# Kernel tuning notes

Hardware: AMD Instinct MI355X
Metric: run time of the kernel (lower is better)

Reference implementation:

```python
import jax, jax.numpy as jnp
import numpy as np
import math

B = 128      # bandwidth
BATCH = 2048 # flat batch (samples x channels)


def _dlt_weights(Bv):
    # Driscoll-Healy quadrature weights, length 2B
    k = np.arange(2 * Bv)
    p = np.arange(Bv)
    C = 2.0 / Bv * np.sin(np.pi * (2 * k + 1) / (4.0 * Bv))
    S = np.sin(np.outer(2 * k + 1, 2 * p + 1) * np.pi / (4.0 * Bv))  # [2B,B]
    return C * (S @ (1.0 / (2 * p + 1)))


def _idct_matrix(N):
    k = np.arange(N)[:, None]
    n = np.arange(N)[None, :]
    DI = np.cos(np.pi * n * (k + 0.5) / N)
    DI[:, 0] *= np.sqrt(1.0 / N)
    DI[:, 1:] *= np.sqrt(2.0 / N)
    return DI


def _idst_matrix(N):
    k = np.arange(N)[:, None]
    n = np.arange(N)[None, :]
    DI = np.sin(np.pi * (n + 1) * (k + 0.5) / N)
    DI[:, N - 1] = (-1.0) ** np.arange(N)
    DI[:, :N - 1] *= np.sqrt(2.0 / N)
    DI[:, N - 1] *= np.sqrt(1.0 / N)
    return DI


def _little_half(Bv):
    # Wigner little-d at beta=pi/2 via 3-term recurrence (vectorized over m,n)
    Bm1 = Bv - 1
    s2 = np.sqrt(2.0)
    d = np.zeros((Bv, 2 * Bv - 1, 2 * Bv - 1))
    d[0, Bm1, Bm1] = 1.0
    d[1, Bm1 - 1, Bm1 - 1] = 0.5
    d[1, Bm1 - 1, Bm1] = 1.0 / s2
    d[1, Bm1 - 1, Bm1 + 1] = 0.5
    d[1, Bm1, Bm1 - 1] = -1.0 / s2
    d[1, Bm1, Bm1 + 1] = 1.0 / s2
    d[1, Bm1 + 1, Bm1 - 1] = 0.5
    d[1, Bm1 + 1, Bm1] = -1.0 / s2
    d[1, Bm1 + 1, Bm1 + 1] = 0.5
    for l in range(2, Bv):
        m = np.arange(l).astype(np.float64)
        M, Nn = np.meshgrid(m, m, indexing='ij')
        denom = (l - 1.0) * np.sqrt((l - M) * (l + M) * (l - Nn) * (l + Nn))
        c1 = (1.0 - 2.0 * l) * M * Nn / denom
        c2 = -l * np.sqrt(((l - 1.0) ** 2 - M ** 2) * ((l - 1.0) ** 2 - Nn ** 2)) / denom
        d[l, Bm1:Bm1 + l, Bm1:Bm1 + l] = (c1 * d[l - 1, Bm1:Bm1 + l, Bm1:Bm1 + l]
                                          + c2 * d[l - 2, Bm1:Bm1 + l, Bm1:Bm1 + l])
        mm = np.arange(l + 1)
        lnV = np.array([0.5 * (math.lgamma(2 * l + 1) - math.lgamma(l + mi + 1)
                               - math.lgamma(l - mi + 1)) - l * math.log(2.0) for mi in mm])
        v = np.exp(lnV)
        d[l, Bm1 + mm, Bm1 + l] = v
        d[l, Bm1 + l, Bm1 + mm] = ((-1.0) ** (l - mm)) * v
        # symmetry fill (write order a1, a2, a3 reproduces torch loop semantics)
        sub = d[l, Bm1:Bm1 + l + 1, Bm1:Bm1 + l + 1].copy()
        M2, N2 = np.meshgrid(np.arange(l + 1), np.arange(l + 1), indexing='ij')
        a1 = ((-1.0) ** (M2 - N2)) * sub
        a2 = ((-1.0) ** (l - N2)) * sub
        a3 = ((-1.0) ** (l + M2)) * sub
        a1[0, 0] = sub[0, 0]
        a2[0, 0] = sub[0, 0]
        a3[0, 0] = sub[0, 0]
        d[l, Bm1 - l:Bm1 + 1, Bm1 - l:Bm1 + 1] = a1[::-1, ::-1]
        d[l, Bm1 - l:Bm1 + 1, Bm1:Bm1 + l + 1] = a2[::-1, :]
        d[l, Bm1:Bm1 + l + 1, Bm1 - l:Bm1 + 1] = a3[:, ::-1]
    return d


def _wigner_coeffs(Bv, d):
    Bm1 = Bv - 1
    N = 2 * Bv
    D = np.zeros((Bv, Bv, N))
    for m in range(Bv):
        for l in range(m, Bv):
            if m % 2 == 0:
                n = np.arange(l + 1)
                c = np.sqrt((2 * l + 1) / 2.0) * np.where(n == 0, np.sqrt(N), np.sqrt(2.0 * N))
                if m % 4 == 2:
                    c = -c
                coeff = c * d[l, n + Bm1, Bm1 - m] * d[l, n + Bm1, Bm1]
                coeff = np.where(np.abs(coeff) > 1e-15, coeff, 0.0)
                D[m, l, :l + 1] = coeff
            else:
                n = np.arange(l)  # n == l gives 0
                if l > 0:
                    c = np.sqrt((2 * l + 1) / 2.0) * np.sqrt(2.0 * N)
                    if m % 4 == 1:
                        c = -c
                    coeff = c * d[l, n + 1 + Bm1, Bm1 - m] * d[l, n + 1 + Bm1, Bm1]
                    coeff = np.where(np.abs(coeff) > 1e-15, coeff, 0.0)
                    D[m, l, :l] = coeff
    return D


def _buffers(Bv):
    N = 2 * Bv
    Wd = np.diag(_dlt_weights(Bv))
    XFc = Wd @ _idct_matrix(N)   # weighted DCT matrix (applied as x @ XFc)
    XFs = Wd @ _idst_matrix(N)   # weighted DST matrix
    D = _wigner_coeffs(Bv, _little_half(Bv))
    cm = ((-1.0) ** (Bv - 1)) * np.sqrt(1.0 / (2.0 * np.pi))  # Cm[B-1] scalar
    return XFc, XFs, D, cm


def setup_inputs() -> dict:
    key = jax.random.key(0)
    psiHat = jax.random.normal(key, (BATCH, B, 2 * B), dtype=jnp.float32)
    XFc, XFs, D, cm = _buffers(B)
    return {
        'psiHat': psiHat,
        'cm': jnp.float32(cm),
        'XFc': jnp.asarray(XFc, dtype=jnp.float32),
        'XFs': jnp.asarray(XFs, dtype=jnp.float32),
        'D': jnp.asarray(D, dtype=jnp.float32),
    }


def reference(psiHat, cm, XFc, XFs, D):
    # psiHat: [batch, B, 2B]; XFc/XFs: [2B, 2B]; D: [B, B, 2B]
    psi = psiHat * cm  # Cm[B-1:] broadcasts as a scalar
    # F.linear with weight = XF.T  ==  x @ XF on the last axis
    psi = psi.at[:, 0::2, :].set(jnp.einsum('bmi,ij->bmj', psi[:, 0::2, :], XFc))
    psi = psi.at[:, 1::2, :].set(jnp.einsum('bmi,ij->bmj', psi[:, 1::2, :], XFs))
    # per-order-m block matmul against Wigner coefficient blocks
    return jnp.einsum('bmi,moi->bmo', psi, D)
```

## Files before the change

kernel.cpp:

```cpp
#include <hip/hip_runtime.h>


typedef __attribute__((ext_vector_type(8))) short short8;
typedef __attribute__((ext_vector_type(4))) float f32x4;

#define NBATCH 2048
#define NM 128
#define NI 256
#define NO 128
#define BPACK_M 32768

#define NSLAB 8
#define SLABROWS 16
#define LDSBUF 16384

#define GLB(p) ((const __attribute__((address_space(1))) void*)(p))
#define LDS(p) ((__attribute__((address_space(3))) void*)(p))

__device__ __forceinline__ unsigned short f2bf(float f) {
  unsigned int u = __builtin_bit_cast(unsigned int, f);
  u += 0x7FFFu + ((u >> 16) & 1u);
  return (unsigned short)(u >> 16);
}

__device__ __forceinline__ short8 cvt8(float4 a, float4 b, float s) {
  short8 v;
  v[0] = (short)f2bf(s * a.x); v[1] = (short)f2bf(s * a.y);
  v[2] = (short)f2bf(s * a.z); v[3] = (short)f2bf(s * a.w);
  v[4] = (short)f2bf(s * b.x); v[5] = (short)f2bf(s * b.y);
  v[6] = (short)f2bf(s * b.z); v[7] = (short)f2bf(s * b.w);
  return v;
}

__global__ __launch_bounds__(256) void e_kernel(
    const float* __restrict__ XFc, const float* __restrict__ XFs,
    const float* __restrict__ D, const float* __restrict__ cmp,
    unsigned short* __restrict__ Bpack)
{
  const int m = blockIdx.x >> 1;
  const int ihalf = blockIdx.x & 1;
  const int tid = threadIdx.x;
  const int lane = tid & 63;
  const int w = tid >> 6;
  const int lr = lane & 15;
  const int lg = lane >> 4;
  const float cm = cmp[0];
  const float* __restrict__ Xp = (m & 1) ? XFs : XFc;
  const float* __restrict__ Dm = D + (size_t)m * (NO * NI);
  const int i0 = ihalf * 128 + w * 32;

  f32x4 acc[2][8];
#pragma unroll
  for (int a = 0; a < 2; a++)
#pragma unroll
    for (int b = 0; b < 8; b++) acc[a][b] = (f32x4)0.f;

  for (int kk = 0; kk < NI; kk += 32) {
    const int kb = kk + lg * 8;
    short8 af[2];
#pragma unroll
    for (int rf = 0; rf < 2; rf++) {
      const float* ap = Xp + (size_t)(i0 + rf * 16 + lr) * NI + kb;
      float4 x0 = *(const float4*)ap;
      float4 x1 = *(const float4*)(ap + 4);
      af[rf] = cvt8(x0, x1, cm);
    }
    short8 bf[8];
#pragma unroll
    for (int cf = 0; cf < 8; cf++) {
      const float* bp = Dm + (size_t)(cf * 16 + lr) * NI + kb;
      float4 x0 = *(const float4*)bp;
      float4 x1 = *(const float4*)(bp + 4);
      bf[cf] = cvt8(x0, x1, 1.0f);
    }
#pragma unroll
    for (int rf = 0; rf < 2; rf++)
#pragma unroll
      for (int cf = 0; cf < 8; cf++)
        acc[rf][cf] = __builtin_amdgcn_mfma_f32_16x16x32_bf16(
            af[rf], bf[cf], acc[rf][cf], 0, 0, 0);
  }

  unsigned short* Bm = Bpack + (size_t)m * BPACK_M;
#pragma unroll
  for (int rf = 0; rf < 2; rf++) {
    const int t = (i0 + rf * 16) >> 5;
    const int L = ((2 * rf + (lg >> 1)) & 3) * 16 + lr;
#pragma unroll
    for (int cf = 0; cf < 8; cf++) {
      ushort4 pk;
      pk.x = f2bf(acc[rf][cf][0]);
      pk.y = f2bf(acc[rf][cf][1]);
      pk.z = f2bf(acc[rf][cf][2]);
      pk.w = f2bf(acc[rf][cf][3]);
      *(ushort4*)(Bm + (size_t)(t * 8 + cf) * 512 + L * 8 + (lg & 1) * 4) = pk;
    }
  }
}

#define SB __builtin_amdgcn_sched_barrier(0)

__global__ __launch_bounds__(256, 4) void fdlt_main(
    const float* __restrict__ psiHat,
    const unsigned short* __restrict__ Bpack,
    float* __restrict__ out)
{
  __shared__ float As_f[2 * SLABROWS * 256];
  __shared__ float Ob_f[SLABROWS * 128];
  const int m = blockIdx.x;
  const int tid = threadIdx.x;
  const int lane = tid & 63;
  const int w = tid >> 6;
  const int bbase = blockIdx.y * (NSLAB * SLABROWS);
  const int lr = lane & 15;
  const int lg = lane >> 4;
  const int cfbase = w * 2;
  char* As = (char*)As_f;
  char* Ob = (char*)Ob_f;

  const unsigned short* __restrict__ Bm = Bpack + (size_t)m * BPACK_M;

  short8 ball[8][2];
#pragma unroll
  for (int t = 0; t < 8; t++)
#pragma unroll
    for (int j = 0; j < 2; j++)
      ball[t][j] = *(const short8*)(
          Bm + (size_t)(t * 8 + cfbase + j) * 512 + lane * 8);

  auto STAGE = [&](int s) {
#pragma unroll
    for (int j = 0; j < 4; j++) {
      const int r = j * 4 + w;
      const int fofs = ((lane ^ (r & 15)) << 2);
      const float* src =
          psiHat + ((size_t)(bbase + s * SLABROWS + r) * NM + m) * NI + fofs;
      __builtin_amdgcn_global_load_lds(GLB(src),
                                       LDS(As + (s & 1) * LDSBUF + r * 1024),
                                       16, 0, 0);
    }
  };

  f32x4 acc[2];

  STAGE(0);
  STAGE(1);
  asm volatile("s_waitcnt vmcnt(4)" ::: "memory");
  SB;
  __builtin_amdgcn_s_barrier();
  SB;

  for (int s = 0; s < NSLAB; s++) {
    const char* Arow = As + (s & 1) * LDSBUF + lr * 1024;
#pragma unroll
    for (int j = 0; j < 2; j++) acc[j] = (f32x4)0.f;
#pragma unroll
    for (int t = 0; t < 8; t++) {
      const int p0 = ((((t * 4 + lg) << 1) ^ lr) << 4);
      float4 x0 = *(const float4*)(Arow + p0);
      float4 x1 = *(const float4*)(Arow + (p0 ^ 16));
      short8 af = cvt8(x0, x1, 1.0f);
#pragma unroll
      for (int j = 0; j < 2; j++)
        acc[j] = __builtin_amdgcn_mfma_f32_16x16x32_bf16(
            af, ball[t][j], acc[j], 0, 0, 0);
    }

#pragma unroll
    for (int j = 0; j < 2; j++) {
      const int u = (cfbase + j) * 4 + (lr >> 2);
#pragma unroll
      for (int r = 0; r < 4; r++) {
        const int row = lg * 4 + r;
        const int p = u ^ (row & 7);
        *(float*)(Ob + row * 512 + p * 16 + (lr & 3) * 4) = acc[j][r];
      }
    }
    asm volatile("s_waitcnt lgkmcnt(0)" ::: "memory");
    SB;
    __builtin_amdgcn_s_barrier();
    SB;

    if (s + 2 < NSLAB) STAGE(s + 2);

#pragma unroll
    for (int i = 0; i < 2; i++) {
      const int c = i * 256 + tid;
      const int row = c >> 5;
      const int u = c & 31;
      const int p = u ^ (row & 7);
      float4 v = *(const float4*)(Ob + row * 512 + p * 16);
      *(float4*)(&out[((size_t)(bbase + s * SLABROWS + row) * NM + m) * NO +
                      u * 4]) = v;
    }
    SB;

    if (s + 1 < NSLAB) {
      if (s + 2 < NSLAB)
        asm volatile("s_waitcnt vmcnt(6)" ::: "memory");
      else
        asm volatile("s_waitcnt vmcnt(2)" ::: "memory");
      SB;
      __builtin_amdgcn_s_barrier();
      SB;
    }
  }
}

extern "C" void kernel_launch(void* const* d_in, const int* in_sizes, int n_in,
                              void* d_out, int out_size, void* d_ws, size_t ws_size,
                              hipStream_t stream) {
  const float* psiHat = (const float*)d_in[0];
  const float* cm     = (const float*)d_in[1];
  const float* XFc    = (const float*)d_in[2];
  const float* XFs    = (const float*)d_in[3];
  const float* D      = (const float*)d_in[4];
  float* out = (float*)d_out;
  unsigned short* Bpack = (unsigned short*)d_ws;

  e_kernel<<<256, 256, 0, stream>>>(XFc, XFs, D, cm, Bpack);
  fdlt_main<<<dim3(NM, NBATCH / (NSLAB * SLABROWS)), 256, 0, stream>>>(
      psiHat, Bpack, out);
}
```

Measured before the change: 106.3 us.

## Retile main kernel over groups of m orders with double-buffered B fragments

Each block now handles 32 batch rows and iterates over 8 consecutive m orders, instead of 128 batch rows for a single m. The packed B fragments for the next m are prefetched into a second register set, while the A slab for m+2 is streamed into LDS. The per-block LDS footprint doubles and occupancy is lowered to 2 blocks per SIMD group. The main gain sought is better locality in psiHat and output accesses, since consecutive m are contiguous in memory, at the cost of reloading B for every 32 rows.

```diff
diff --git a/kernel.cpp b/kernel.cpp
--- a/kernel.cpp
+++ b/kernel.cpp
@@ -10,9 +10,9 @@
 #define NO 128
 #define BPACK_M 32768
 
-#define NSLAB 8
-#define SLABROWS 16
-#define LDSBUF 16384
+#define BROWS 32
+#define MGRP 8
+#define ABUF 32768
 
 #define GLB(p) ((const __attribute__((address_space(1))) void*)(p))
 #define LDS(p) ((__attribute__((address_space(3))) void*)(p))
@@ -100,110 +100,125 @@
 
 #define SB __builtin_amdgcn_sched_barrier(0)
 
-__global__ __launch_bounds__(256, 4) void fdlt_main(
+__global__ __launch_bounds__(256, 2) void fdlt_main(
     const float* __restrict__ psiHat,
     const unsigned short* __restrict__ Bpack,
     float* __restrict__ out)
 {
-  __shared__ float As_f[2 * SLABROWS * 256];
-  __shared__ float Ob_f[SLABROWS * 128];
-  const int m = blockIdx.x;
+  __shared__ float As_f[2 * BROWS * 256];
+  __shared__ float Ob_f[BROWS * 128];
+  const int m0 = blockIdx.x * MGRP;
+  const int b0 = blockIdx.y * BROWS;
   const int tid = threadIdx.x;
   const int lane = tid & 63;
   const int w = tid >> 6;
-  const int bbase = blockIdx.y * (NSLAB * SLABROWS);
   const int lr = lane & 15;
   const int lg = lane >> 4;
   const int cfbase = w * 2;
   char* As = (char*)As_f;
   char* Ob = (char*)Ob_f;
 
-  const unsigned short* __restrict__ Bm = Bpack + (size_t)m * BPACK_M;
-
-  short8 ball[8][2];
-#pragma unroll
-  for (int t = 0; t < 8; t++)
-#pragma unroll
-    for (int j = 0; j < 2; j++)
-      ball[t][j] = *(const short8*)(
-          Bm + (size_t)(t * 8 + cfbase + j) * 512 + lane * 8);
-
-  auto STAGE = [&](int s) {
-#pragma unroll
-    for (int j = 0; j < 4; j++) {
+  auto LOADB = [&](short8 (&bl)[8][2], int ms) {
+    const unsigned short* Bm = Bpack + (size_t)(m0 + ms) * BPACK_M;
+#pragma unroll
+    for (int t = 0; t < 8; t++)
+#pragma unroll
+      for (int j = 0; j < 2; j++)
+        bl[t][j] = *(const short8*)(
+            Bm + (size_t)(t * 8 + cfbase + j) * 512 + lane * 8);
+  };
+
+  auto STAGE = [&](int ms) {
+#pragma unroll
+    for (int j = 0; j < 8; j++) {
       const int r = j * 4 + w;
       const int fofs = ((lane ^ (r & 15)) << 2);
       const float* src =
-          psiHat + ((size_t)(bbase + s * SLABROWS + r) * NM + m) * NI + fofs;
+          psiHat + ((size_t)(b0 + r) * NM + (m0 + ms)) * NI + fofs;
       __builtin_amdgcn_global_load_lds(GLB(src),
-                                       LDS(As + (s & 1) * LDSBUF + r * 1024),
+                                       LDS(As + (ms & 1) * ABUF + r * 1024),
                                        16, 0, 0);
     }
   };
 
-  f32x4 acc[2];
-
-  STAGE(0);
-  STAGE(1);
-  asm volatile("s_waitcnt vmcnt(4)" ::: "memory");
-  SB;
-  __builtin_amdgcn_s_barrier();
-  SB;
-
-  for (int s = 0; s < NSLAB; s++) {
-    const char* Arow = As + (s & 1) * LDSBUF + lr * 1024;
-#pragma unroll
-    for (int j = 0; j < 2; j++) acc[j] = (f32x4)0.f;
+  short8 ballA[8][2], ballB[8][2];
+  f32x4 acc[2][2];
+
+  auto SLAB = [&](int ms, short8 (&cur)[8][2], short8 (&nxt)[8][2]) {
+#pragma unroll
+    for (int rg = 0; rg < 2; rg++)
+#pragma unroll
+      for (int j = 0; j < 2; j++) acc[rg][j] = (f32x4)0.f;
 #pragma unroll
     for (int t = 0; t < 8; t++) {
       const int p0 = ((((t * 4 + lg) << 1) ^ lr) << 4);
-      float4 x0 = *(const float4*)(Arow + p0);
-      float4 x1 = *(const float4*)(Arow + (p0 ^ 16));
-      short8 af = cvt8(x0, x1, 1.0f);
-#pragma unroll
-      for (int j = 0; j < 2; j++)
-        acc[j] = __builtin_amdgcn_mfma_f32_16x16x32_bf16(
-            af, ball[t][j], acc[j], 0, 0, 0);
-    }
-
-#pragma unroll
-    for (int j = 0; j < 2; j++) {
-      const int u = (cfbase + j) * 4 + (lr >> 2);
-#pragma unroll
-      for (int r = 0; r < 4; r++) {
-        const int row = lg * 4 + r;
-        const int p = u ^ (row & 7);
-        *(float*)(Ob + row * 512 + p * 16 + (lr & 3) * 4) = acc[j][r];
+#pragma unroll
+      for (int rg = 0; rg < 2; rg++) {
+        const char* Arow = As + (ms & 1) * ABUF + (rg * 16 + lr) * 1024;
+        float4 x0 = *(const float4*)(Arow + p0);
+        float4 x1 = *(const float4*)(Arow + (p0 ^ 16));
+        short8 af = cvt8(x0, x1, 1.0f);
+#pragma unroll
+        for (int j = 0; j < 2; j++)
+          acc[rg][j] = __builtin_amdgcn_mfma_f32_16x16x32_bf16(
+              af, cur[t][j], acc[rg][j], 0, 0, 0);
       }
     }
+
+#pragma unroll
+    for (int rg = 0; rg < 2; rg++)
+#pragma unroll
+      for (int j = 0; j < 2; j++) {
+        const int u = (cfbase + j) * 4 + (lr >> 2);
+#pragma unroll
+        for (int r = 0; r < 4; r++) {
+          const int row = rg * 16 + lg * 4 + r;
+          const int p = u ^ (row & 7);
+          *(float*)(Ob + row * 512 + p * 16 + (lr & 3) * 4) = acc[rg][j][r];
+        }
+      }
     asm volatile("s_waitcnt lgkmcnt(0)" ::: "memory");
     SB;
     __builtin_amdgcn_s_barrier();
     SB;
 
-    if (s + 2 < NSLAB) STAGE(s + 2);
-
-#pragma unroll
-    for (int i = 0; i < 2; i++) {
+    if (ms + 1 < MGRP) LOADB(nxt, ms + 1);
+    if (ms + 2 < MGRP) STAGE(ms + 2);
+
+#pragma unroll
+    for (int i = 0; i < 4; i++) {
       const int c = i * 256 + tid;
       const int row = c >> 5;
       const int u = c & 31;
       const int p = u ^ (row & 7);
       float4 v = *(const float4*)(Ob + row * 512 + p * 16);
-      *(float4*)(&out[((size_t)(bbase + s * SLABROWS + row) * NM + m) * NO +
-                      u * 4]) = v;
+      *(float4*)(&out[((size_t)(b0 + row) * NM + (m0 + ms)) * NO + u * 4]) = v;
     }
     SB;
 
-    if (s + 1 < NSLAB) {
-      if (s + 2 < NSLAB)
-        asm volatile("s_waitcnt vmcnt(6)" ::: "memory");
+    if (ms + 1 < MGRP) {
+      if (ms + 2 < MGRP)
+        asm volatile("s_waitcnt vmcnt(12)" ::: "memory");
       else
-        asm volatile("s_waitcnt vmcnt(2)" ::: "memory");
+        asm volatile("s_waitcnt vmcnt(4)" ::: "memory");
       SB;
       __builtin_amdgcn_s_barrier();
       SB;
     }
+  };
+
+  LOADB(ballA, 0);
+  STAGE(0);
+  STAGE(1);
+  asm volatile("s_waitcnt vmcnt(8)" ::: "memory");
+  SB;
+  __builtin_amdgcn_s_barrier();
+  SB;
+
+#pragma unroll
+  for (int ms = 0; ms < MGRP; ms += 2) {
+    SLAB(ms, ballA, ballB);
+    SLAB(ms + 1, ballB, ballA);
   }
 }
 
@@ -219,6 +234,6 @@
   unsigned short* Bpack = (unsigned short*)d_ws;
 
   e_kernel<<<256, 256, 0, stream>>>(XFc, XFs, D, cm, Bpack);
-  fdlt_main<<<dim3(NM, NBATCH / (NSLAB * SLABROWS)), 256, 0, stream>>>(
+  fdlt_main<<<dim3(NM / MGRP, NBATCH / BROWS), 256, 0, stream>>>(
       psiHat, Bpack, out);
 }
```

After: 123.4 us. 1.16x slower.
